# Kernel optimization log

Measured on AMD Instinct MI355X. Metric: run time of the kernel, lower is better.

Reference implementation:

```python
import jax, jax.numpy as jnp
import numpy as np

# ---- model dims (match torch para_dict) ----
B, F1, F2, F_OUT = 16, 32, 64, 10
B0, B1, B2 = 32, 16, 8           # bandwidths: input / layer1 / layer2
M1, M2 = 2 * B1 - 1, 2 * B2 - 1  # padded spectral width over signed m
NUM_POINTS = 1
EPS = 1e-5

_LF = np.concatenate([[0.0], np.cumsum(np.log(np.arange(1.0, 200.0)))])  # _LF[i] = log(i!)

def _betas(b):
    return np.pi * (2.0 * np.arange(2 * b) + 1.0) / (4.0 * b)

def _quad_weights(b):
    # Driscoll-Healy quadrature weights on the 2b beta grid
    beta = _betas(b)
    k = np.arange(b)[:, None]
    s = np.sum(np.sin((2 * k + 1) * beta[None, :]) / (2 * k + 1), axis=0)
    return (2.0 / b) * np.sin(beta) * s

def _wig(l, m, n, betas):
    # small Wigner d^l_{m,n}(beta), vectorized over betas (float64)
    kmin, kmax = max(0, m - n), min(l + m, l - n)
    k = np.arange(kmin, kmax + 1)
    pref = 0.5 * (_LF[l + m] + _LF[l - m] + _LF[l + n] + _LF[l - n])
    coef = (-1.0) ** k * np.exp(pref - _LF[k] - _LF[l + m - k] - _LF[l - n - k] - _LF[n - m + k])
    cb, sb = np.cos(betas / 2)[:, None], np.sin(betas / 2)[:, None]
    return (coef * cb ** (2 * l + m - n - 2 * k) * sb ** (n - m + 2 * k)).sum(1)

def _build():
    b0g, b1g, b2g = _betas(B0), _betas(B1), _betas(B2)
    w0, w1q = _quad_weights(B0), _quad_weights(B1)
    d1f = np.zeros((B1, 2 * B0, M1))        # S2 forward: w_j * d^l_{m0}(beta_j)
    d1i = np.zeros((B1, 2 * B1, M1, M1))    # SO3 inverse at layer-1 grid, * (2l+1)
    d2f = np.zeros((B2, 2 * B1, M2, M2))    # SO3 forward at layer-1 grid, * w_j
    d2i = np.zeros((B2, 2 * B2, M2, M2))    # SO3 inverse at layer-2 grid, * (2l+1)
    mask1, mask2 = np.zeros((B1, M1)), np.zeros((B2, M2, M2))
    for l in range(B1):
        o = (B1 - 1) - l
        mask1[l, o:o + 2 * l + 1] = 1.0
        for m in range(-l, l + 1):
            d1f[l, :, o + m + l] = w0 * _wig(l, m, 0, b0g)
            for n in range(-l, l + 1):
                d1i[l, :, o + m + l, o + n + l] = (2 * l + 1) * _wig(l, m, n, b1g)
    for l in range(B2):
        o = (B2 - 1) - l
        mask2[l, o:o + 2 * l + 1, o:o + 2 * l + 1] = 1.0
        for m in range(-l, l + 1):
            for n in range(-l, l + 1):
                d2f[l, :, o + m + l, o + n + l] = w1q * _wig(l, m, n, b1g)
                d2i[l, :, o + m + l, o + n + l] = (2 * l + 1) * _wig(l, m, n, b2g)
    return d1f, d1i, d2f, d2i, mask1, mask2

_d1f, _d1i, _d2f, _d2i, _m1, _m2 = _build()
D1F = jnp.asarray(_d1f, jnp.float32)
D1I = jnp.asarray(_d1i, jnp.float32)
D2F = jnp.asarray(_d2f, jnp.float32)
D2I = jnp.asarray(_d2i, jnp.float32)
MASK1 = jnp.asarray(_m1, jnp.float32)
MASK2 = jnp.asarray(_m2, jnp.float32)
IDX1 = jnp.asarray(np.arange(-(B1 - 1), B1) % (2 * B0), jnp.int32)
IDXG1 = jnp.asarray(np.arange(-(B1 - 1), B1) % (2 * B1), jnp.int32)
IDX2 = jnp.asarray(np.arange(-(B2 - 1), B2) % (2 * B1), jnp.int32)
IDXG2 = jnp.asarray(np.arange(-(B2 - 1), B2) % (2 * B2), jnp.int32)

def _so3_ifft(yh, d_inv, idx, n):
    # yh: [B,F,L,M,M] SO3 spectrum -> signal [B,F,2b,2b,2b] on (beta, alpha, gamma)
    f = jnp.einsum('ljmn,bflmn->bfjmn', d_inv, yh)
    z = jnp.zeros(f.shape[:3] + (n, n), dtype=f.dtype)
    z = z.at[..., idx[:, None], idx[None, :]].set(f)
    return jnp.real(jnp.fft.ifft2(z, axes=(-2, -1))) * (n * n)

def _forward(x, w1r, w1i, w2r, w2i, conv3_w, conv3_b, bn_gamma, bn_beta, fc_w, fc_b):
    # ---- S2 convolution (b_in=B0 -> b_out=B1) ----
    xm = jnp.take(jnp.fft.fft(x, axis=-1), IDX1, axis=-1)      # alpha FFT, signed m  [B,1,2B0,M1]
    xh = jnp.einsum('ljm,bcjm->bclm', D1F, xm)                 # S2 FFT  [B,1,B1,M1]
    w1 = (w1r + 1j * w1i) * MASK1                              # [1,F1,B1,M1]
    yh1 = jnp.einsum('bclm,cfln->bflmn', xh, jnp.conj(w1))     # outer product -> SO3 spectrum
    r1 = jax.nn.relu(_so3_ifft(yh1, D1I, IDXG1, 2 * B1))       # [B,F1,2B1,2B1,2B1]
    # ---- SO3 convolution (b_in=B1 -> b_out=B2) ----
    xf2 = jnp.fft.fft2(r1, axes=(-2, -1))                      # over (alpha, gamma)
    xmn = xf2[..., IDX2[:, None], IDX2[None, :]]               # [B,F1,2B1,M2,M2]
    xh2 = jnp.einsum('ljmn,bcjmn->bclmn', D2F, xmn)            # SO3 FFT [B,F1,B2,M2,M2]
    w2 = (w2r + 1j * w2i) * MASK2                              # [F1,F2,B2,M2,M2]
    yh2 = jnp.einsum('bclmk,cflnk->bflmn', xh2, jnp.conj(w2))  # x_hat @ w_hat^H per l
    r2 = jax.nn.relu(_so3_ifft(yh2, D2I, IDXG2, 2 * B2))       # [B,F2,2B2,2B2,2B2]
    # ---- head: conv1d -> relu -> batchnorm(train) -> linear ----
    feat = r2[:, :, 0, 0, 0].reshape(B, 1, NUM_POINTS * F2)
    c3 = jax.lax.conv_general_dilated(feat, conv3_w, (1,), 'VALID',
                                      dimension_numbers=('NCH', 'OIH', 'NCH'))
    r3 = jax.nn.relu(c3 + conv3_b[None, :, None])              # [B,10,57]
    mu = jnp.mean(r3, axis=(0, 2), keepdims=True)
    var = jnp.mean((r3 - mu) ** 2, axis=(0, 2), keepdims=True)
    bn = bn_gamma[None, :, None] * (r3 - mu) * jax.lax.rsqrt(var + EPS) + bn_beta[None, :, None]
    return bn.reshape(B, -1) @ fc_w.T + fc_b

def setup_inputs():
    key = jax.random.key(0)
    ks = jax.random.split(key, 8)
    f = jnp.float32
    return {
        "x": jax.random.normal(ks[0], (B, 1, 2 * B0, 2 * B0), f),
        "w1r": 0.1 * jax.random.normal(ks[1], (1, F1, B1, M1), f),
        "w1i": 0.1 * jax.random.normal(ks[2], (1, F1, B1, M1), f),
        "w2r": 0.05 * jax.random.normal(ks[3], (F1, F2, B2, M2, M2), f),
        "w2i": 0.05 * jax.random.normal(ks[4], (F1, F2, B2, M2, M2), f),
        "conv3_w": 0.3 * jax.random.normal(ks[5], (10, 1, 8), f),
        "conv3_b": jnp.zeros((10,), f),
        "bn_gamma": jnp.ones((10,), f),
        "bn_beta": jnp.zeros((10,), f),
        "fc_w": 0.05 * jax.random.normal(ks[6], (F_OUT, 10 * (NUM_POINTS * F2 - 8 + 1)), f),
        "fc_b": jnp.zeros((F_OUT,), f),
    }

def reference(x, w1r, w1i, w2r, w2i, conv3_w, conv3_b, bn_gamma, bn_beta, fc_w, fc_b):
    return _forward(x, w1r, w1i, w2r, w2i, conv3_w, conv3_b, bn_gamma, bn_beta, fc_w, fc_b)
```

## Files before the change

### kernel.cpp

```cpp
#include <hip/hip_runtime.h>
#include <math.h>

#ifndef M_PI
#define M_PI 3.14159265358979323846
#endif

#define OFF_TRIG 708
#define OFF_D1F 900
#define OFF_D1I 32644
#define OFF_D2F 540548
#define OFF_S2  598148
#define OFF_XH  599948
#define OFF_XMN 615820
#define OFF_U   7988620
#define OFF_FEAT 9831820

static __device__ __forceinline__ int iabs_(int v) { return v < 0 ? -v : v; }

static __device__ __forceinline__ double powi_d(double x, int e) {
    double r = 1.0;
    while (e) { if (e & 1) r *= x; x *= x; e >>= 1; }
    return r;
}

__global__ __launch_bounds__(256) void k0a_tables(float* __restrict__ ws) {
    double* T = (double*)ws;
    int t = threadIdx.x;
    __shared__ double lg[64];
    if (t < 64) lg[t] = (t == 0) ? 0.0 : log((double)t);
    __syncthreads();
    if (t == 0) {
        double s = 0.0;
        for (int i = 0; i < 64; ++i) { s += lg[i]; T[i] = s; }
    }
    if (t < 64) {
        double beta = M_PI * (2.0 * t + 1.0) / 128.0;
        double s = 0.0;
        for (int k = 0; k < 32; ++k) s += sin((2.0 * k + 1.0) * beta) / (2.0 * k + 1.0);
        T[64 + t] = 2.0 / 32.0 * sin(beta) * s;
        T[160 + t] = cos(0.5 * beta);
        T[224 + t] = sin(0.5 * beta);
    }
    if (t >= 64 && t < 96) {
        int j = t - 64;
        double beta = M_PI * (2.0 * j + 1.0) / 64.0;
        double s = 0.0;
        for (int k = 0; k < 16; ++k) s += sin((2.0 * k + 1.0) * beta) / (2.0 * k + 1.0);
        T[128 + j] = 2.0 / 16.0 * sin(beta) * s;
        T[288 + j] = cos(0.5 * beta);
        T[320 + j] = sin(0.5 * beta);
    }
    if (t == 96) {
        T[352] = cos(M_PI / 64.0);
        T[353] = sin(M_PI / 64.0);
    }
    float2* F = (float2*)(ws + OFF_TRIG);
    if (t < 32) {
        double a = 2.0 * M_PI * (double)t / 32.0;
        F[t] = make_float2((float)cos(a), (float)sin(a));
    }
    if (t >= 128 && t < 192) {
        int i = t - 128;
        double a = 2.0 * M_PI * (double)i / 64.0;
        F[32 + i] = make_float2((float)cos(a), (float)sin(a));
    }
    for (int i = t; i < 1024; i += 256) ws[OFF_FEAT + i] = 0.f;
}

__device__ double wig_fast(int l, int m, int n, double cb, double sb, const double* LF) {
    int kmin = max(0, m - n), kmax = min(l + m, l - n);
    if (kmax < kmin) return 0.0;
    double lc = 0.5 * (LF[l + m] + LF[l - m] + LF[l + n] + LF[l - n])
              - LF[kmin] - LF[l + m - kmin] - LF[l - n - kmin] - LF[n - m + kmin];
    double t = exp(lc) * powi_d(cb, 2 * l + m - n - 2 * kmin)
                       * powi_d(sb, n - m + 2 * kmin);
    if (kmin & 1) t = -t;
    double ratio = (sb * sb) / (cb * cb);
    double s = t;
    for (int k = kmin; k < kmax; ++k) {
        t *= -(((double)(l + m - k) * (double)(l - n - k)) /
               ((double)(k + 1) * (double)(n - m + k + 1))) * ratio;
        s += t;
    }
    return s;
}

__global__ __launch_bounds__(256) void k0_consts(float* __restrict__ ws) {
    const double* T = (const double*)ws;
    __shared__ double LF[64];
    int tid = threadIdx.x;
    if (tid < 64) LF[tid] = T[tid];
    __syncthreads();
    int gid = blockIdx.x * 256 + tid;
    if (gid >= 599048) return;

    if (gid < 31744) {
        int mh = gid % 31, j = (gid / 31) % 64, l = gid / (31 * 64);
        int m = mh - 15;
        double v = 0.0;
        if (iabs_(m) <= l)
            v = T[64 + j] * wig_fast(l, m, 0, T[160 + j], T[224 + j], LF);
        ws[OFF_D1F + gid] = (float)v;
    } else if (gid < 539648) {
        int r = gid - 31744;
        int nh = r & 31;
        int l  = (r >> 5) & 15;
        int mh = (r >> 9) % 31;
        int j  = r / (512 * 31);
        int m = mh - 15, n = nh - 15;
        double v = 0.0;
        if (nh < 31 && iabs_(m) <= l && iabs_(n) <= l)
            v = (2.0 * l + 1.0) * wig_fast(l, m, n, T[288 + j], T[320 + j], LF);
        ws[OFF_D1I + r] = (float)v;
    } else if (gid < 597248) {
        int r = gid - 539648;
        int l = r & 7;
        int pq = (r >> 3) % 225;
        int j = r / 1800;
        int mh = pq / 15, nh = pq % 15;
        int m = mh - 7, n = nh - 7;
        double v = 0.0;
        if (iabs_(m) <= l && iabs_(n) <= l)
            v = T[128 + j] * wig_fast(l, m, n, T[288 + j], T[320 + j], LF);
        ws[OFF_D2F + r] = (float)v;
    } else {
        int r = gid - 597248;
        int nh = r % 15, mh = (r / 15) % 15, l = r / 225;
        int m = mh - 7, n = nh - 7;
        double v = 0.0;
        if (iabs_(m) <= l && iabs_(n) <= l)
            v = (2.0 * l + 1.0) * wig_fast(l, m, n, T[352], T[353], LF);
        ws[OFF_S2 + r] = (float)v;
    }
}

__global__ __launch_bounds__(256) void k1_xh(const float* __restrict__ x,
                                             const float* __restrict__ ws,
                                             float2* __restrict__ xh) {
    __shared__ float  xs[64 * 64];
    __shared__ float2 xm[64 * 8];
    __shared__ float2 cs64[64];
    int c = blockIdx.x, b = blockIdx.y, tid = threadIdx.x;
    int mh0 = c * 8;
    int cnt = min(8, 31 - mh0);
    for (int i = tid; i < 4096; i += 256) xs[i] = x[b * 4096 + i];
    if (tid < 64) cs64[tid] = ((const float2*)(ws + OFF_TRIG))[32 + tid];
    __syncthreads();
    for (int i = tid; i < 512; i += 256) {
        int j = i >> 3, mi = i & 7;
        if (mi < cnt) {
            int mu = mh0 + mi - 15;
            float re = 0.f, im = 0.f;
            for (int t = 0; t < 64; ++t) {
                float2 w = cs64[(mu * t) & 63];
                float xv = xs[j * 64 + t];
                re += xv * w.x;
                im -= xv * w.y;
            }
            xm[i] = make_float2(re, im);
        }
    }
    __syncthreads();
    const float* D1F = ws + OFF_D1F;
    if (tid < 128) {
        int l = tid >> 3, mi = tid & 7;
        if (mi < cnt) {
            int mh = mh0 + mi;
            float re = 0.f, im = 0.f;
            for (int j = 0; j < 64; ++j) {
                float d = D1F[(l * 64 + j) * 31 + mh];
                float2 v = xm[j * 8 + mi];
                re += d * v.x;
                im += d * v.y;
            }
            xh[b * 496 + l * 31 + mh] = make_float2(re, im);
        }
    }
}

__global__ __launch_bounds__(256) void k2_planes(const float* __restrict__ w1r,
                                                 const float* __restrict__ w1i,
                                                 const float* __restrict__ ws,
                                                 float2* __restrict__ xmn) {
    __shared__ char ar[16896];
    __shared__ float2 cs[32];
    float2* As  = (float2*)ar;
    float2* Wc  = (float2*)(ar + 4096);
    float2* f1  = (float2*)(ar + 8448);
    float2* fH  = (float2*)ar;
    float2* tls = (float2*)(ar + 4608);
    float*  ssb = (float*)(ar + 9216);
    float2* gg  = (float2*)ar;

    int j = blockIdx.x, f = blockIdx.y, b = blockIdx.z;
    int tid = threadIdx.x;
    const float2* xh = (const float2*)(ws + OFF_XH);

    if (tid < 32) cs[tid] = ((const float2*)(ws + OFF_TRIG))[tid];
    for (int i = tid; i < 496; i += 256) As[i] = xh[b * 496 + i];
    for (int i = tid; i < 512; i += 256) {
        int l = i >> 5, nh = i & 31;
        float mask = (nh < 31 && iabs_(nh - 15) <= l) ? 1.0f : 0.0f;
        int src = f * 496 + l * 31 + min(nh, 30);
        Wc[i] = make_float2(w1r[src] * mask, -w1i[src] * mask);
    }
    __syncthreads();
    {
        int mrow = tid >> 3;
        int nh0 = (tid & 7) * 4;
        if (mrow < 31) {
            int l0 = iabs_(mrow - 15);
            float2 a0 = {0,0}, a1 = {0,0}, a2 = {0,0}, a3 = {0,0};
            const float* Dbase = ws + OFF_D1I + ((j * 31 + mrow) * 16) * 32 + nh0;
            for (int l = l0; l < 16; ++l) {
                float2 a = As[l * 31 + mrow];
                float4 w01 = *(const float4*)(Wc + l * 32 + nh0);
                float4 w23 = *(const float4*)(Wc + l * 32 + nh0 + 2);
                float4 d = *(const float4*)(Dbase + l * 32);
                float t;
                t = a.x*w01.x - a.y*w01.y; a0.x += d.x*t;
                t = a.x*w01.y + a.y*w01.x; a0.y += d.x*t;
                t = a.x*w01.z - a.y*w01.w; a1.x += d.y*t;
                t = a.x*w01.w + a.y*w01.z; a1.y += d.y*t;
                t = a.x*w23.x - a.y*w23.y; a2.x += d.z*t;
                t = a.x*w23.y + a.y*w23.x; a2.y += d.z*t;
                t = a.x*w23.z - a.y*w23.w; a3.x += d.w*t;
                t = a.x*w23.w + a.y*w23.z; a3.y += d.w*t;
            }
            float2* fr = f1 + mrow * 34 + nh0;
            fr[0] = a0; fr[1] = a1; fr[2] = a2; fr[3] = a3;
        }
    }
    __syncthreads();
    for (int i = tid; i < 512; i += 256) {
        int mm = i >> 5, nh = i & 31;
        float2 v = make_float2(0.f, 0.f);
        if (nh < 31) {
            float2 a = f1[(mm + 15) * 34 + nh];
            float2 bb = f1[(15 - mm) * 34 + (30 - nh)];
            v = make_float2(0.5f * (a.x + bb.x), 0.5f * (a.y - bb.y));
        }
        fH[mm * 34 + nh] = v;
    }
    __syncthreads();
    if (tid < 128) {
        int mm = tid >> 3, v0 = tid & 7;
        const float2* frow = fH + mm * 34;
        float2 a0 = {0,0}, a1 = {0,0}, a2 = {0,0}, a3 = {0,0};
        for (int nb = 0; nb < 32; nb += 4) {
            float4 q01 = *(const float4*)(frow + nb);
            float4 q23 = *(const float4*)(frow + nb + 2);
            {
                float2 w = cs[((nb - 15) * v0) & 31];
                float px = q01.x*w.x - q01.y*w.y, py = q01.x*w.y + q01.y*w.x;
                a0.x += px; a0.y += py;  a1.x -= py; a1.y += px;
                a2.x -= px; a2.y -= py;  a3.x += py; a3.y -= px;
            }
            {
                float2 w = cs[((nb - 14) * v0) & 31];
                float px = q01.z*w.x - q01.w*w.y, py = q01.z*w.y + q01.w*w.x;
                a0.x += px; a0.y += py;  a1.x -= px; a1.y -= py;
                a2.x += px; a2.y += py;  a3.x -= px; a3.y -= py;
            }
            {
                float2 w = cs[((nb - 13) * v0) & 31];
                float px = q23.x*w.x - q23.y*w.y, py = q23.x*w.y + q23.y*w.x;
                a0.x += px; a0.y += py;  a1.x += py; a1.y -= px;
                a2.x -= px; a2.y -= py;  a3.x -= py; a3.y += px;
            }
            {
                float2 w = cs[((nb - 12) * v0) & 31];
                float px = q23.z*w.x - q23.w*w.y, py = q23.z*w.y + q23.w*w.x;
                a0.x += px; a0.y += py;  a1.x += px; a1.y += py;
                a2.x += px; a2.y += py;  a3.x += px; a3.y += py;
            }
        }
        float2* trow = tls + mm * 33;
        trow[v0] = a0; trow[v0 + 8] = a1; trow[v0 + 16] = a2; trow[v0 + 24] = a3;
    } else if (tid < 161) {
        tls[16 * 33 + (tid - 128)] = make_float2(0.f, 0.f);
    }
    __syncthreads();
    {
        int v = tid & 31, u0 = tid >> 5;
        float s0 = 0, s1 = 0, s2 = 0, s3 = 0;
        for (int mb = 0; mb < 4; ++mb) {
            int r1 = mb * 4 + 1;
            {
                float2 tv = tls[r1 * 33 + v];       float2 w = cs[(r1 * u0) & 31];
                float qx = tv.x*w.x - tv.y*w.y, qy = tv.x*w.y + tv.y*w.x;
                s0 += qx; s1 -= qy; s2 -= qx; s3 += qy;
            }
            {
                float2 tv = tls[(r1 + 1) * 33 + v]; float2 w = cs[((r1 + 1) * u0) & 31];
                float qx = tv.x*w.x - tv.y*w.y;
                s0 += qx; s1 -= qx; s2 += qx; s3 -= qx;
            }
            {
                float2 tv = tls[(r1 + 2) * 33 + v]; float2 w = cs[((r1 + 2) * u0) & 31];
                float qx = tv.x*w.x - tv.y*w.y, qy = tv.x*w.y + tv.y*w.x;
                s0 += qx; s1 += qy; s2 -= qx; s3 -= qy;
            }
            {
                float2 tv = tls[(r1 + 3) * 33 + v]; float2 w = cs[((r1 + 3) * u0) & 31];
                float qx = tv.x*w.x - tv.y*w.y;
                s0 += qx; s1 += qx; s2 += qx; s3 += qx;
            }
        }
        float t0x = tls[v].x;
        ssb[u0 * 33 + v]        = fmaxf(t0x + 2.f * s0, 0.f);
        ssb[(u0 + 8) * 33 + v]  = fmaxf(t0x + 2.f * s1, 0.f);
        ssb[(u0 + 16) * 33 + v] = fmaxf(t0x + 2.f * s2, 0.f);
        ssb[(u0 + 24) * 33 + v] = fmaxf(t0x + 2.f * s3, 0.f);
    }
    __syncthreads();
    {
        int u = tid >> 3, q = tid & 7;
        int qm = q & 3;
        float r1 = (qm == 0) ? 1.f : (qm == 2 ? -1.f : 0.f);
        float r2 = (qm & 1) ? -1.f : 1.f;
        float i1 = (qm == 1) ? -1.f : (qm == 3 ? 1.f : 0.f);
        float gx = 0.f, gy = 0.f;
        const float* srow = ssb + u * 33;
        for (int vb = 0; vb < 8; ++vb) {
            float s0 = srow[vb], s1 = srow[vb + 8], s2 = srow[vb + 16], s3 = srow[vb + 24];
            float zre = s0 + r1 * s1 + r2 * s2 + r1 * s3;
            float zim = i1 * (s1 - s3);
            float2 w = cs[(q * vb) & 31];
            gx += zre * w.x + zim * w.y;
            gy += zim * w.x - zre * w.y;
        }
        gg[u * 15 + 7 + q] = make_float2(gx, gy);
        if (q) gg[u * 15 + 7 - q] = make_float2(gx, -gy);
    }
    __syncthreads();
    if (tid < 113) {
        int ph, qh;
        if (tid < 105) { ph = 8 + tid / 15; qh = tid % 15; }
        else           { ph = 7; qh = 7 + (tid - 105); }
        int p = ph - 7;
        float hx = 0.f, hy = 0.f;
        for (int u = 0; u < 32; ++u) {
            float2 gv = gg[u * 15 + qh];
            float2 w = cs[(-(p * u)) & 31];
            hx += gv.x * w.x - gv.y * w.y;
            hy += gv.x * w.y + gv.y * w.x;
        }
        float2* outp = xmn + ((size_t)((b * 32 + f) * 32 + j)) * 225;
        outp[ph * 15 + qh] = make_float2(hx, hy);
        if (ph > 7 || qh > 7)
            outp[(14 - ph) * 15 + (14 - qh)] = make_float2(hx, -hy);
    }
}

__global__ __launch_bounds__(256) void k34_U(const float* __restrict__ ws,
                                             const float2* __restrict__ xmn,
                                             float2* __restrict__ U) {
    __shared__ float2 xh2s[1800];
    __shared__ float  S2s[1800];
    int bc = blockIdx.x, tid = threadIdx.x;

    for (int i = tid; i < 1800; i += 256) S2s[i] = ws[OFF_S2 + i];

    float2 acc[8];
#pragma unroll
    for (int l = 0; l < 8; ++l) acc[l] = make_float2(0.f, 0.f);
    if (tid < 225) {
        const float2* xp = xmn + (size_t)bc * 7200;
        const float4* dw = (const float4*)(ws + OFF_D2F);
        for (int j = 0; j < 32; ++j) {
            float2 xv = xp[j * 225 + tid];
            float4 dA = dw[(j * 225 + tid) * 2];
            float4 dB = dw[(j * 225 + tid) * 2 + 1];
            acc[0].x += dA.x * xv.x; acc[0].y += dA.x * xv.y;
            acc[1].x += dA.y * xv.x; acc[1].y += dA.y * xv.y;
            acc[2].x += dA.z * xv.x; acc[2].y += dA.z * xv.y;
            acc[3].x += dA.w * xv.x; acc[3].y += dA.w * xv.y;
            acc[4].x += dB.x * xv.x; acc[4].y += dB.x * xv.y;
            acc[5].x += dB.y * xv.x; acc[5].y += dB.y * xv.y;
            acc[6].x += dB.z * xv.x; acc[6].y += dB.z * xv.y;
            acc[7].x += dB.w * xv.x; acc[7].y += dB.w * xv.y;
        }
#pragma unroll
        for (int l = 0; l < 8; ++l) xh2s[l * 225 + tid] = acc[l];
    }
    __syncthreads();

    for (int idx = tid; idx < 1800; idx += 256) {
        int l = idx / 225;
        int rem = idx - l * 225;
        int n = rem / 15, k = rem - n * 15;
        float2 a = make_float2(0.f, 0.f);
        for (int m = 0; m < 15; ++m) {
            float s = S2s[(l * 15 + m) * 15 + n];
            float2 v = xh2s[l * 225 + m * 15 + k];
            a.x += s * v.x;
            a.y += s * v.y;
        }
        U[(size_t)bc * 1800 + idx] = a;
    }
}

__global__ __launch_bounds__(256) void k5_feat(const float* __restrict__ w2r,
                                               const float* __restrict__ w2i,
                                               const float2* __restrict__ U,
                                               float* __restrict__ feat) {
    __shared__ char ar[57600];
    float2* Us  = (float2*)ar;
    float2* Wsh = (float2*)(ar + 28800);
    int bx = blockIdx.x;
    int c = bx >> 5, l = (bx >> 2) & 7, fc = bx & 3;
    int tid = threadIdx.x;

    for (int i = tid; i < 3600; i += 256) {
        int b = i / 225, t = i - b * 225;
        Us[i] = U[(size_t)(b * 32 + c) * 1800 + l * 225 + t];
    }
    for (int i = tid; i < 3600; i += 256) {
        int f = fc * 16 + i / 225;
        int t = i % 225;
        int n = t / 15, k = t - n * 15;
        bool valid = (iabs_(n - 7) <= l) && (iabs_(k - 7) <= l);
        int wi = ((c * 64 + f) * 8 + l) * 225 + t;
        Wsh[i] = valid ? make_float2(w2r[wi], w2i[wi]) : make_float2(0.f, 0.f);
    }
    __syncthreads();
    int b = tid >> 4, fl = tid & 15;
    float accv = 0.f;
    const float2* up = Us + b * 225;
    const float2* wp = Wsh + fl * 225;
    for (int t = 0; t < 225; ++t)
        accv += up[t].x * wp[t].x + up[t].y * wp[t].y;
    atomicAdd(&feat[b * 64 + fc * 16 + fl], accv);
}

__global__ __launch_bounds__(640) void k6_head(const float* __restrict__ feat,
                                               const float* __restrict__ w3,
                                               const float* __restrict__ b3,
                                               const float* __restrict__ gamma,
                                               const float* __restrict__ beta,
                                               const float* __restrict__ fcw,
                                               const float* __restrict__ fcb,
                                               float* __restrict__ out) {
    __shared__ float fL[1024];
    __shared__ float w3L[80];
    __shared__ float b3L[10];
    __shared__ float r3[9120];
    __shared__ float scaleL[10], shiftL[10];
    int tid = threadIdx.x;
    for (int i = tid; i < 1024; i += 640) fL[i] = fmaxf(feat[i], 0.f);
    if (tid < 80) w3L[tid] = w3[tid];
    if (tid >= 80 && tid < 90) b3L[tid - 80] = b3[tid - 80];
    __syncthreads();
    for (int i = tid; i < 9120; i += 640) {
        int ch = i / 912;
        int r = i % 912;
        int b = r / 57, pos = r % 57;
        float acc = b3L[ch];
#pragma unroll
        for (int t = 0; t < 8; ++t) acc += fL[b * 64 + pos + t] * w3L[ch * 8 + t];
        r3[ch * 912 + r] = fmaxf(acc, 0.0f);
    }
    __syncthreads();
    int wave = tid >> 6, lane = tid & 63;
    if (wave < 10) {
        float s = 0.f, s2 = 0.f;
        for (int i = lane; i < 912; i += 64) {
            float v = r3[wave * 912 + i];
            s += v;
            s2 += v * v;
        }
        for (int off = 32; off > 0; off >>= 1) {
            s += __shfl_down(s, off);
            s2 += __shfl_down(s2, off);
        }
        if (lane == 0) {
            float mu = s / 912.0f;
            float var = s2 / 912.0f - mu * mu;
            float sc = gamma[wave] * rsqrtf(var + 1e-5f);
            scaleL[wave] = sc;
            shiftL[wave] = beta[wave] - mu * sc;
        }
    }
    __syncthreads();
    {
        int pair = tid >> 2, sub = tid & 3;
        int b = pair / 10, o = pair % 10;
        float acc = 0.f;
        for (int idx = sub; idx < 570; idx += 4) {
            int ch = idx / 57, pos = idx - ch * 57;
            acc += (r3[ch * 912 + b * 57 + pos] * scaleL[ch] + shiftL[ch])
                   * fcw[o * 570 + idx];
        }
        acc += __shfl_down(acc, 2);
        acc += __shfl_down(acc, 1);
        if (sub == 0) out[b * 10 + o] = acc + fcb[o];
    }
}

extern "C" void kernel_launch(void* const* d_in, const int* in_sizes, int n_in,
                              void* d_out, int out_size, void* d_ws, size_t ws_size,
                              hipStream_t stream) {
    const float* x   = (const float*)d_in[0];
    const float* w1r = (const float*)d_in[1];
    const float* w1i = (const float*)d_in[2];
    const float* w2r = (const float*)d_in[3];
    const float* w2i = (const float*)d_in[4];
    const float* c3w = (const float*)d_in[5];
    const float* c3b = (const float*)d_in[6];
    const float* bng = (const float*)d_in[7];
    const float* bnb = (const float*)d_in[8];
    const float* fcw = (const float*)d_in[9];
    const float* fcb = (const float*)d_in[10];
    float* ws = (float*)d_ws;
    float* out = (float*)d_out;

    hipLaunchKernelGGL(k0a_tables, dim3(1), dim3(256), 0, stream, ws);
    hipLaunchKernelGGL(k0_consts, dim3(2341), dim3(256), 0, stream, ws);
    hipLaunchKernelGGL(k1_xh, dim3(4, 16), dim3(256), 0, stream, x, ws,
                       (float2*)(ws + OFF_XH));
    hipLaunchKernelGGL(k2_planes, dim3(32, 32, 16), dim3(256), 0, stream, w1r, w1i, ws,
                       (float2*)(ws + OFF_XMN));
    hipLaunchKernelGGL(k34_U, dim3(512), dim3(256), 0, stream, ws,
                       (const float2*)(ws + OFF_XMN), (float2*)(ws + OFF_U));
    hipLaunchKernelGGL(k5_feat, dim3(1024), dim3(256), 0, stream, w2r, w2i,
                       (const float2*)(ws + OFF_U), ws + OFF_FEAT);
    hipLaunchKernelGGL(k6_head, dim3(1), dim3(640), 0, stream, ws + OFF_FEAT,
                       c3w, c3b, bng, bnb, fcw, fcb, out);
}
```

Before: 321.4 us.

## Vectorize complex math with packed float2 ops and radix-4 DFT butterflies

Rewrites the complex multiply-accumulates in the plane and spectral kernels using 2-wide vector types, so the compiler can emit packed FP32 FMA instructions. The weights are pre-split into two arrays and the twiddles are stored as (c,s,-s,c), which removes the sign shuffles. The DFT loops accumulate four phase-class partial sums and combine them with a final radix-4 butterfly instead of updating four accumulators per term. The feature kernel pads its shared rows to 226 entries so it can use 16-byte vector loads with two accumulators. The cost is more shared memory and extra LDS reads for the duplicated weight array.

```diff
diff --git a/kernel.cpp b/kernel.cpp
--- a/kernel.cpp
+++ b/kernel.cpp
@@ -15,7 +15,14 @@
 #define OFF_U   7988620
 #define OFF_FEAT 9831820
 
+typedef float v2f __attribute__((ext_vector_type(2)));
+typedef float v4f __attribute__((ext_vector_type(4)));
+
 static __device__ __forceinline__ int iabs_(int v) { return v < 0 ? -v : v; }
+
+static __device__ __forceinline__ v2f mkv2(float a, float b) {
+    v2f r; r.x = a; r.y = b; return r;
+}
 
 static __device__ __forceinline__ double powi_d(double x, int e) {
     double r = 1.0;
@@ -182,11 +189,12 @@
                                                  const float* __restrict__ w1i,
                                                  const float* __restrict__ ws,
                                                  float2* __restrict__ xmn) {
-    __shared__ char ar[16896];
-    __shared__ float2 cs[32];
+    __shared__ char ar[20736];
+    __shared__ v4f cs4s[32];
     float2* As  = (float2*)ar;
-    float2* Wc  = (float2*)(ar + 4096);
-    float2* f1  = (float2*)(ar + 8448);
+    float2* Wa  = (float2*)(ar + 4096);
+    float2* Wb  = (float2*)(ar + 8192);
+    float2* f1  = (float2*)(ar + 12288);
     float2* fH  = (float2*)ar;
     float2* tls = (float2*)(ar + 4608);
     float*  ssb = (float*)(ar + 9216);
@@ -196,13 +204,19 @@
     int tid = threadIdx.x;
     const float2* xh = (const float2*)(ws + OFF_XH);
 
-    if (tid < 32) cs[tid] = ((const float2*)(ws + OFF_TRIG))[tid];
+    if (tid < 32) {
+        float2 w = ((const float2*)(ws + OFF_TRIG))[tid];
+        v4f c; c.x = w.x; c.y = w.y; c.z = -w.y; c.w = w.x;
+        cs4s[tid] = c;
+    }
     for (int i = tid; i < 496; i += 256) As[i] = xh[b * 496 + i];
     for (int i = tid; i < 512; i += 256) {
         int l = i >> 5, nh = i & 31;
         float mask = (nh < 31 && iabs_(nh - 15) <= l) ? 1.0f : 0.0f;
         int src = f * 496 + l * 31 + min(nh, 30);
-        Wc[i] = make_float2(w1r[src] * mask, -w1i[src] * mask);
+        float wr = w1r[src] * mask, wi = w1i[src] * mask;
+        Wa[i] = make_float2(wr, -wi);
+        Wb[i] = make_float2(wi, wr);
     }
     __syncthreads();
     {
@@ -210,25 +224,26 @@
         int nh0 = (tid & 7) * 4;
         if (mrow < 31) {
             int l0 = iabs_(mrow - 15);
-            float2 a0 = {0,0}, a1 = {0,0}, a2 = {0,0}, a3 = {0,0};
+            v2f a0 = {0.f, 0.f}, a1 = {0.f, 0.f}, a2 = {0.f, 0.f}, a3 = {0.f, 0.f};
             const float* Dbase = ws + OFF_D1I + ((j * 31 + mrow) * 16) * 32 + nh0;
             for (int l = l0; l < 16; ++l) {
                 float2 a = As[l * 31 + mrow];
-                float4 w01 = *(const float4*)(Wc + l * 32 + nh0);
-                float4 w23 = *(const float4*)(Wc + l * 32 + nh0 + 2);
-                float4 d = *(const float4*)(Dbase + l * 32);
-                float t;
-                t = a.x*w01.x - a.y*w01.y; a0.x += d.x*t;
-                t = a.x*w01.y + a.y*w01.x; a0.y += d.x*t;
-                t = a.x*w01.z - a.y*w01.w; a1.x += d.y*t;
-                t = a.x*w01.w + a.y*w01.z; a1.y += d.y*t;
-                t = a.x*w23.x - a.y*w23.y; a2.x += d.z*t;
-                t = a.x*w23.y + a.y*w23.x; a2.y += d.z*t;
-                t = a.x*w23.z - a.y*w23.w; a3.x += d.w*t;
-                t = a.x*w23.w + a.y*w23.z; a3.y += d.w*t;
+                v4f wA01 = *(const v4f*)(Wa + l * 32 + nh0);
+                v4f wA23 = *(const v4f*)(Wa + l * 32 + nh0 + 2);
+                v4f wB01 = *(const v4f*)(Wb + l * 32 + nh0);
+                v4f wB23 = *(const v4f*)(Wb + l * 32 + nh0 + 2);
+                v4f d = *(const v4f*)(Dbase + l * 32);
+                v2f p;
+                p = a.x * wA01.xy + a.y * wB01.xy;  a0 += d.x * p;
+                p = a.x * wA01.zw + a.y * wB01.zw;  a1 += d.y * p;
+                p = a.x * wA23.xy + a.y * wB23.xy;  a2 += d.z * p;
+                p = a.x * wA23.zw + a.y * wB23.zw;  a3 += d.w * p;
             }
             float2* fr = f1 + mrow * 34 + nh0;
-            fr[0] = a0; fr[1] = a1; fr[2] = a2; fr[3] = a3;
+            v4f s01; s01.x = a0.x; s01.y = a0.y; s01.z = a1.x; s01.w = a1.y;
+            v4f s23; s23.x = a2.x; s23.y = a2.y; s23.z = a3.x; s23.w = a3.y;
+            *(v4f*)(fr)     = s01;
+            *(v4f*)(fr + 2) = s23;
         }
     }
     __syncthreads();
@@ -246,67 +261,56 @@
     if (tid < 128) {
         int mm = tid >> 3, v0 = tid & 7;
         const float2* frow = fH + mm * 34;
-        float2 a0 = {0,0}, a1 = {0,0}, a2 = {0,0}, a3 = {0,0};
+        v2f S0 = {0.f, 0.f}, S1 = {0.f, 0.f}, S2 = {0.f, 0.f}, S3 = {0.f, 0.f};
+        int ci = (17 * v0) & 31;
+#pragma unroll
         for (int nb = 0; nb < 32; nb += 4) {
-            float4 q01 = *(const float4*)(frow + nb);
-            float4 q23 = *(const float4*)(frow + nb + 2);
-            {
-                float2 w = cs[((nb - 15) * v0) & 31];
-                float px = q01.x*w.x - q01.y*w.y, py = q01.x*w.y + q01.y*w.x;
-                a0.x += px; a0.y += py;  a1.x -= py; a1.y += px;
-                a2.x -= px; a2.y -= py;  a3.x += py; a3.y -= px;
-            }
-            {
-                float2 w = cs[((nb - 14) * v0) & 31];
-                float px = q01.z*w.x - q01.w*w.y, py = q01.z*w.y + q01.w*w.x;
-                a0.x += px; a0.y += py;  a1.x -= px; a1.y -= py;
-                a2.x += px; a2.y += py;  a3.x -= px; a3.y -= py;
-            }
-            {
-                float2 w = cs[((nb - 13) * v0) & 31];
-                float px = q23.x*w.x - q23.y*w.y, py = q23.x*w.y + q23.y*w.x;
-                a0.x += px; a0.y += py;  a1.x += py; a1.y -= px;
-                a2.x -= px; a2.y -= py;  a3.x -= py; a3.y += px;
-            }
-            {
-                float2 w = cs[((nb - 12) * v0) & 31];
-                float px = q23.z*w.x - q23.w*w.y, py = q23.z*w.y + q23.w*w.x;
-                a0.x += px; a0.y += py;  a1.x += px; a1.y += py;
-                a2.x += px; a2.y += py;  a3.x += px; a3.y += py;
-            }
-        }
+            v4f fa = *(const v4f*)(frow + nb);
+            v4f fb = *(const v4f*)(frow + nb + 2);
+            v4f w;
+            w = cs4s[ci]; ci = (ci + v0) & 31;
+            S1 += fa.x * w.xy; S1 += fa.y * w.zw;
+            w = cs4s[ci]; ci = (ci + v0) & 31;
+            S2 += fa.z * w.xy; S2 += fa.w * w.zw;
+            w = cs4s[ci]; ci = (ci + v0) & 31;
+            S3 += fb.x * w.xy; S3 += fb.y * w.zw;
+            w = cs4s[ci]; ci = (ci + v0) & 31;
+            S0 += fb.z * w.xy; S0 += fb.w * w.zw;
+        }
+        v2f E = S0 + S2, F = S0 - S2, G = S1 + S3, H = S1 - S3;
+        v2f A0 = E + G, A2 = E - G;
+        v2f iH = mkv2(-H.y, H.x);
+        v2f A1 = F + iH, A3 = F - iH;
         float2* trow = tls + mm * 33;
-        trow[v0] = a0; trow[v0 + 8] = a1; trow[v0 + 16] = a2; trow[v0 + 24] = a3;
+        trow[v0]      = make_float2(A0.x, A0.y);
+        trow[v0 + 8]  = make_float2(A1.x, A1.y);
+        trow[v0 + 16] = make_float2(A2.x, A2.y);
+        trow[v0 + 24] = make_float2(A3.x, A3.y);
     } else if (tid < 161) {
         tls[16 * 33 + (tid - 128)] = make_float2(0.f, 0.f);
     }
     __syncthreads();
     {
         int v = tid & 31, u0 = tid >> 5;
-        float s0 = 0, s1 = 0, s2 = 0, s3 = 0;
-        for (int mb = 0; mb < 4; ++mb) {
-            int r1 = mb * 4 + 1;
-            {
-                float2 tv = tls[r1 * 33 + v];       float2 w = cs[(r1 * u0) & 31];
-                float qx = tv.x*w.x - tv.y*w.y, qy = tv.x*w.y + tv.y*w.x;
-                s0 += qx; s1 -= qy; s2 -= qx; s3 += qy;
-            }
-            {
-                float2 tv = tls[(r1 + 1) * 33 + v]; float2 w = cs[((r1 + 1) * u0) & 31];
-                float qx = tv.x*w.x - tv.y*w.y;
-                s0 += qx; s1 -= qx; s2 += qx; s3 -= qx;
-            }
-            {
-                float2 tv = tls[(r1 + 2) * 33 + v]; float2 w = cs[((r1 + 2) * u0) & 31];
-                float qx = tv.x*w.x - tv.y*w.y, qy = tv.x*w.y + tv.y*w.x;
-                s0 += qx; s1 += qy; s2 -= qx; s3 -= qy;
-            }
-            {
-                float2 tv = tls[(r1 + 3) * 33 + v]; float2 w = cs[((r1 + 3) * u0) & 31];
-                float qx = tv.x*w.x - tv.y*w.y;
-                s0 += qx; s1 += qx; s2 += qx; s3 += qx;
-            }
-        }
+        v2f Z0 = {0.f, 0.f}, Z1 = {0.f, 0.f}, Z2 = {0.f, 0.f}, Z3 = {0.f, 0.f};
+        int ci = u0;
+#pragma unroll
+        for (int mb = 1; mb <= 16; mb += 4) {
+            float2 tv; v4f w;
+            tv = tls[mb * 33 + v];        w = cs4s[ci]; ci = (ci + u0) & 31;
+            Z1 += tv.x * w.xy; Z1 += tv.y * w.zw;
+            tv = tls[(mb + 1) * 33 + v];  w = cs4s[ci]; ci = (ci + u0) & 31;
+            Z2 += tv.x * w.xy; Z2 += tv.y * w.zw;
+            tv = tls[(mb + 2) * 33 + v];  w = cs4s[ci]; ci = (ci + u0) & 31;
+            Z3 += tv.x * w.xy; Z3 += tv.y * w.zw;
+            tv = tls[(mb + 3) * 33 + v];  w = cs4s[ci]; ci = (ci + u0) & 31;
+            Z0 += tv.x * w.xy; Z0 += tv.y * w.zw;
+        }
+        float E = Z0.x + Z2.x, F = Z0.x - Z2.x;
+        float G = Z1.x + Z3.x;
+        float Hy = Z1.y - Z3.y;
+        float s0 = E + G, s2 = E - G;
+        float s1 = F - Hy, s3 = F + Hy;
         float t0x = tls[v].x;
         ssb[u0 * 33 + v]        = fmaxf(t0x + 2.f * s0, 0.f);
         ssb[(u0 + 8) * 33 + v]  = fmaxf(t0x + 2.f * s1, 0.f);
@@ -320,18 +324,19 @@
         float r1 = (qm == 0) ? 1.f : (qm == 2 ? -1.f : 0.f);
         float r2 = (qm & 1) ? -1.f : 1.f;
         float i1 = (qm == 1) ? -1.f : (qm == 3 ? 1.f : 0.f);
-        float gx = 0.f, gy = 0.f;
+        v2f g = {0.f, 0.f};
         const float* srow = ssb + u * 33;
+        int ci = 0;
+#pragma unroll
         for (int vb = 0; vb < 8; ++vb) {
             float s0 = srow[vb], s1 = srow[vb + 8], s2 = srow[vb + 16], s3 = srow[vb + 24];
-            float zre = s0 + r1 * s1 + r2 * s2 + r1 * s3;
+            float zre = (s0 + r2 * s2) + r1 * (s1 + s3);
             float zim = i1 * (s1 - s3);
-            float2 w = cs[(q * vb) & 31];
-            gx += zre * w.x + zim * w.y;
-            gy += zim * w.x - zre * w.y;
-        }
-        gg[u * 15 + 7 + q] = make_float2(gx, gy);
-        if (q) gg[u * 15 + 7 - q] = make_float2(gx, -gy);
+            v4f w = cs4s[ci]; ci = (ci - q) & 31;
+            g += zre * w.xy; g += zim * w.zw;
+        }
+        gg[u * 15 + 7 + q] = make_float2(g.x, g.y);
+        if (q) gg[u * 15 + 7 - q] = make_float2(g.x, -g.y);
     }
     __syncthreads();
     if (tid < 113) {
@@ -339,17 +344,18 @@
         if (tid < 105) { ph = 8 + tid / 15; qh = tid % 15; }
         else           { ph = 7; qh = 7 + (tid - 105); }
         int p = ph - 7;
-        float hx = 0.f, hy = 0.f;
+        v2f h = {0.f, 0.f};
+        int ci = 0;
+#pragma unroll 8
         for (int u = 0; u < 32; ++u) {
             float2 gv = gg[u * 15 + qh];
-            float2 w = cs[(-(p * u)) & 31];
-            hx += gv.x * w.x - gv.y * w.y;
-            hy += gv.x * w.y + gv.y * w.x;
+            v4f w = cs4s[ci]; ci = (ci - p) & 31;
+            h += gv.x * w.xy; h += gv.y * w.zw;
         }
         float2* outp = xmn + ((size_t)((b * 32 + f) * 32 + j)) * 225;
-        outp[ph * 15 + qh] = make_float2(hx, hy);
+        outp[ph * 15 + qh] = make_float2(h.x, h.y);
         if (ph > 7 || qh > 7)
-            outp[(14 - ph) * 15 + (14 - qh)] = make_float2(hx, -hy);
+            outp[(14 - ph) * 15 + (14 - qh)] = make_float2(h.x, -h.y);
     }
 }
 
@@ -362,27 +368,27 @@
 
     for (int i = tid; i < 1800; i += 256) S2s[i] = ws[OFF_S2 + i];
 
-    float2 acc[8];
-#pragma unroll
-    for (int l = 0; l < 8; ++l) acc[l] = make_float2(0.f, 0.f);
+    v2f a0 = {0.f,0.f}, a1 = {0.f,0.f}, a2 = {0.f,0.f}, a3 = {0.f,0.f};
+    v2f a4 = {0.f,0.f}, a5 = {0.f,0.f}, a6 = {0.f,0.f}, a7 = {0.f,0.f};
     if (tid < 225) {
         const float2* xp = xmn + (size_t)bc * 7200;
-        const float4* dw = (const float4*)(ws + OFF_D2F);
+        const v4f* dw = (const v4f*)(ws + OFF_D2F);
         for (int j = 0; j < 32; ++j) {
-            float2 xv = xp[j * 225 + tid];
-            float4 dA = dw[(j * 225 + tid) * 2];
-            float4 dB = dw[(j * 225 + tid) * 2 + 1];
-            acc[0].x += dA.x * xv.x; acc[0].y += dA.x * xv.y;
-            acc[1].x += dA.y * xv.x; acc[1].y += dA.y * xv.y;
-            acc[2].x += dA.z * xv.x; acc[2].y += dA.z * xv.y;
-            acc[3].x += dA.w * xv.x; acc[3].y += dA.w * xv.y;
-            acc[4].x += dB.x * xv.x; acc[4].y += dB.x * xv.y;
-            acc[5].x += dB.y * xv.x; acc[5].y += dB.y * xv.y;
-            acc[6].x += dB.z * xv.x; acc[6].y += dB.z * xv.y;
-            acc[7].x += dB.w * xv.x; acc[7].y += dB.w * xv.y;
-        }
-#pragma unroll
-        for (int l = 0; l < 8; ++l) xh2s[l * 225 + tid] = acc[l];
+            float2 xvf = xp[j * 225 + tid];
+            v2f xv = mkv2(xvf.x, xvf.y);
+            v4f dA = dw[(j * 225 + tid) * 2];
+            v4f dB = dw[(j * 225 + tid) * 2 + 1];
+            a0 += dA.x * xv; a1 += dA.y * xv; a2 += dA.z * xv; a3 += dA.w * xv;
+            a4 += dB.x * xv; a5 += dB.y * xv; a6 += dB.z * xv; a7 += dB.w * xv;
+        }
+        xh2s[0 * 225 + tid] = make_float2(a0.x, a0.y);
+        xh2s[1 * 225 + tid] = make_float2(a1.x, a1.y);
+        xh2s[2 * 225 + tid] = make_float2(a2.x, a2.y);
+        xh2s[3 * 225 + tid] = make_float2(a3.x, a3.y);
+        xh2s[4 * 225 + tid] = make_float2(a4.x, a4.y);
+        xh2s[5 * 225 + tid] = make_float2(a5.x, a5.y);
+        xh2s[6 * 225 + tid] = make_float2(a6.x, a6.y);
+        xh2s[7 * 225 + tid] = make_float2(a7.x, a7.y);
     }
     __syncthreads();
 
@@ -390,14 +396,13 @@
         int l = idx / 225;
         int rem = idx - l * 225;
         int n = rem / 15, k = rem - n * 15;
-        float2 a = make_float2(0.f, 0.f);
+        v2f a = {0.f, 0.f};
         for (int m = 0; m < 15; ++m) {
             float s = S2s[(l * 15 + m) * 15 + n];
-            float2 v = xh2s[l * 225 + m * 15 + k];
-            a.x += s * v.x;
-            a.y += s * v.y;
-        }
-        U[(size_t)bc * 1800 + idx] = a;
+            float2 vf = xh2s[l * 225 + m * 15 + k];
+            a += s * mkv2(vf.x, vf.y);
+        }
+        U[(size_t)bc * 1800 + idx] = make_float2(a.x, a.y);
     }
 }
 
@@ -405,32 +410,41 @@
                                                const float* __restrict__ w2i,
                                                const float2* __restrict__ U,
                                                float* __restrict__ feat) {
-    __shared__ char ar[57600];
+    __shared__ char ar[57856];
     float2* Us  = (float2*)ar;
-    float2* Wsh = (float2*)(ar + 28800);
+    float2* Wsh = (float2*)(ar + 28928);
     int bx = blockIdx.x;
     int c = bx >> 5, l = (bx >> 2) & 7, fc = bx & 3;
     int tid = threadIdx.x;
 
     for (int i = tid; i < 3600; i += 256) {
         int b = i / 225, t = i - b * 225;
-        Us[i] = U[(size_t)(b * 32 + c) * 1800 + l * 225 + t];
+        Us[b * 226 + t] = U[(size_t)(b * 32 + c) * 1800 + l * 225 + t];
     }
     for (int i = tid; i < 3600; i += 256) {
-        int f = fc * 16 + i / 225;
-        int t = i % 225;
+        int fr = i / 225;
+        int f = fc * 16 + fr;
+        int t = i - fr * 225;
         int n = t / 15, k = t - n * 15;
         bool valid = (iabs_(n - 7) <= l) && (iabs_(k - 7) <= l);
         int wi = ((c * 64 + f) * 8 + l) * 225 + t;
-        Wsh[i] = valid ? make_float2(w2r[wi], w2i[wi]) : make_float2(0.f, 0.f);
+        Wsh[fr * 226 + t] = valid ? make_float2(w2r[wi], w2i[wi]) : make_float2(0.f, 0.f);
+    }
+    if (tid < 16) {
+        Us[tid * 226 + 225]  = make_float2(0.f, 0.f);
+        Wsh[tid * 226 + 225] = make_float2(0.f, 0.f);
     }
     __syncthreads();
     int b = tid >> 4, fl = tid & 15;
-    float accv = 0.f;
-    const float2* up = Us + b * 225;
-    const float2* wp = Wsh + fl * 225;
-    for (int t = 0; t < 225; ++t)
-        accv += up[t].x * wp[t].x + up[t].y * wp[t].y;
+    const v4f* up = (const v4f*)(Us + b * 226);
+    const v4f* wp = (const v4f*)(Wsh + fl * 226);
+    v2f acc2 = {0.f, 0.f};
+    for (int t = 0; t < 113; ++t) {
+        v4f u4 = up[t], w4 = wp[t];
+        acc2 += u4.xy * w4.xy;
+        acc2 += u4.zw * w4.zw;
+    }
+    float accv = acc2.x + acc2.y;
     atomicAdd(&feat[b * 64 + fc * 16 + fl], accv);
 }
 
```

Measured after the change: 315.4 us. About the same (-1.9%).
